# Optimization experiments

Hardware: AMD Instinct MI355X
Metric: run time of the kernel (lower is better)

## Reference

```python
import jax, jax.numpy as jnp
import numpy as np

N_NODES = 100000
N_EDGES = 1600000
IN_CH = 128
HID = 128   # 2 * out_channels
OUT_CH = 64


def setup_inputs() -> dict:
    key = jax.random.key(0)
    k1, k2, k3, k4, k5, k6 = jax.random.split(key, 6)
    x = jax.random.normal(k1, (N_NODES, IN_CH), dtype=jnp.float32)
    edge_index = jax.random.randint(k2, (2, N_EDGES), 0, N_NODES, dtype=jnp.int64)
    W1 = jax.random.normal(k3, (IN_CH, HID), dtype=jnp.float32) / np.sqrt(IN_CH)
    b1 = jax.random.normal(k4, (HID,), dtype=jnp.float32) * 0.01
    W2 = jax.random.normal(k5, (HID, OUT_CH), dtype=jnp.float32) / np.sqrt(HID)
    b2 = jax.random.normal(k6, (OUT_CH,), dtype=jnp.float32) * 0.01
    return {"x": x, "edge_index": edge_index, "W1": W1, "b1": b1, "W2": W2, "b2": b2}


def _gcn_layer(x, src, dst, norm, W, b, n_nodes):
    # GCNConv: linear transform, then normalized scatter-add aggregation + bias
    h = x @ W                                   # [N, d_out]
    msg = h[src] * norm[:, None]                # gather + edge normalize, [E+N, d_out]
    out = jax.ops.segment_sum(msg, dst, num_segments=n_nodes)
    return out + b


def reference(x, edge_index, W1, b1, W2, b2):
    n = x.shape[0]
    loop = jnp.arange(n, dtype=edge_index.dtype)
    # add self-loops (PyG GCNConv default)
    src = jnp.concatenate([edge_index[0], loop])
    dst = jnp.concatenate([edge_index[1], loop])
    # symmetric normalization deg^-1/2[src] * deg^-1/2[dst]
    deg = jax.ops.segment_sum(jnp.ones_like(dst, x.dtype), dst, num_segments=n)
    dinv = jnp.where(deg > 0, jax.lax.rsqrt(deg), 0.0)
    norm = dinv[src] * dinv[dst]

    h = jax.nn.relu(_gcn_layer(x, src, dst, norm, W1, b1, n))
    out = jax.nn.relu(_gcn_layer(h, src, dst, norm, W2, b2, n))
    return out
```

## Files before the change

### kernel.cpp

```cpp
#include <hip/hip_runtime.h>
#include <hip/hip_fp16.h>

typedef _Float16 f16x8 __attribute__((ext_vector_type(8)));
typedef float f32x4 __attribute__((ext_vector_type(4)));

#define BSH 9
#define BSZ 512
#define CAP 12288

__global__ __launch_bounds__(256) void passA(const int* __restrict__ ei,
                                             int* __restrict__ bcount, int E, int NB) {
  __shared__ int hist[256];
  int t = threadIdx.x;
  hist[t] = 0;
  __syncthreads();
  for (int e = blockIdx.x * 256 + t; e < E; e += gridDim.x * 256)
    atomicAdd(&hist[ei[E + e] >> BSH], 1);
  __syncthreads();
  if (t < NB && hist[t]) atomicAdd(&bcount[t], hist[t]);
}

__global__ __launch_bounds__(256) void scanB(const int* __restrict__ bcount,
                                             int* __restrict__ bstart,
                                             int* __restrict__ bfill, int NB, int E) {
  __shared__ int s[256];
  int t = threadIdx.x;
  int v = (t < NB) ? bcount[t] : 0;
  s[t] = v;
  __syncthreads();
  for (int off = 1; off < 256; off <<= 1) {
    int add = (t >= off) ? s[t - off] : 0;
    __syncthreads();
    s[t] += add;
    __syncthreads();
  }
  if (t < NB) {
    int ex = s[t] - v;
    bstart[t] = ex;
    bfill[t] = ex;
  }
  if (t == 0) bstart[NB] = E;
}

template <int NC, int NWC, bool IN_F16, bool SCALE>
__device__ __forceinline__ void gemm_mfma_body(
    const void* __restrict__ Xv, const float* __restrict__ W,
    const float* __restrict__ dinv, _Float16* __restrict__ G, int nrows, int bid,
    _Float16* Bs) {
  int t = threadIdx.x;
  {
    int n = t % NC;
    int kh = (t / NC) * (NC / 2);
    constexpr int NBLK = (NC / 2) / 8;
#pragma unroll
    for (int b = 0; b < NBLK; ++b) {
      f16x8 tmp;
#pragma unroll
      for (int j = 0; j < 8; ++j)
        tmp[j] = (_Float16)W[(size_t)(kh + b * 8 + j) * NC + n];
      *(f16x8*)(&Bs[n * 136 + kh + b * 8]) = tmp;
    }
  }
  __syncthreads();

  int w = t >> 6, lane = t & 63;
  int m = lane & 15, q = lane >> 4;
  int wr = (w / NWC) * 64, wc = (w % NWC) * 64;
  int row0 = bid * ((4 / NWC) * 64);

  f32x4 acc[4][4];
#pragma unroll
  for (int rt = 0; rt < 4; ++rt)
#pragma unroll
    for (int ct = 0; ct < 4; ++ct)
#pragma unroll
      for (int qq = 0; qq < 4; ++qq) acc[rt][ct][qq] = 0.f;

#pragma unroll
  for (int kc = 0; kc < 4; ++kc) {
    int kbase = kc * 32 + q * 8;
    f16x8 af[4];
#pragma unroll
    for (int rt = 0; rt < 4; ++rt) {
      int row = row0 + wr + rt * 16 + m;
      if constexpr (IN_F16) {
        f16x8 a = {0, 0, 0, 0, 0, 0, 0, 0};
        if (row < nrows) a = *(const f16x8*)((const _Float16*)Xv + (size_t)row * 128 + kbase);
        af[rt] = a;
      } else {
        float4 x0 = {0, 0, 0, 0}, x1 = {0, 0, 0, 0};
        if (row < nrows) {
          const float* Xf = (const float*)Xv;
          x0 = *(const float4*)(Xf + (size_t)row * 128 + kbase);
          x1 = *(const float4*)(Xf + (size_t)row * 128 + kbase + 4);
        }
        f16x8 a;
        a[0] = (_Float16)x0.x; a[1] = (_Float16)x0.y;
        a[2] = (_Float16)x0.z; a[3] = (_Float16)x0.w;
        a[4] = (_Float16)x1.x; a[5] = (_Float16)x1.y;
        a[6] = (_Float16)x1.z; a[7] = (_Float16)x1.w;
        af[rt] = a;
      }
    }
    f16x8 bf[4];
#pragma unroll
    for (int ct = 0; ct < 4; ++ct) {
      int n = wc + ct * 16 + m;
      bf[ct] = *(f16x8*)(&Bs[n * 136 + kbase]);
    }
#pragma unroll
    for (int rt = 0; rt < 4; ++rt)
#pragma unroll
      for (int ct = 0; ct < 4; ++ct)
        acc[rt][ct] = __builtin_amdgcn_mfma_f32_16x16x32_f16(af[rt], bf[ct],
                                                             acc[rt][ct], 0, 0, 0);
  }
#pragma unroll
  for (int rt = 0; rt < 4; ++rt) {
#pragma unroll
    for (int r = 0; r < 4; ++r) {
      int row = row0 + wr + rt * 16 + q * 4 + r;
      if (row < nrows) {
        float d = SCALE ? dinv[row] : 1.f;
#pragma unroll
        for (int ct = 0; ct < 4; ++ct) {
          int col = wc + ct * 16 + m;
          G[(size_t)row * NC + col] = (_Float16)(acc[rt][ct][r] * d);
        }
      }
    }
  }
}

__global__ __launch_bounds__(256) void fused_gemm_passB(
    const float* __restrict__ X, const float* __restrict__ W1,
    _Float16* __restrict__ G, int nrows, int GB,
    const int* __restrict__ ei, int* __restrict__ bfill,
    unsigned int* __restrict__ pairs, int E, int PB) {
  __shared__ char smem[128 * 136 * 2];
  int g = blockIdx.x;
  int M2 = 2 * (GB < PB ? GB : PB);
  bool is_gemm;
  int bid;
  if (g < M2) { is_gemm = (g & 1) == 0; bid = g >> 1; }
  else        { is_gemm = (GB > PB);    bid = g - M2 + (GB < PB ? GB : PB); }
  if (is_gemm) {
    gemm_mfma_body<128, 2, false, false>(X, W1, nullptr, G, nrows, bid,
                                         (_Float16*)smem);
  } else {
    int* hist = (int*)smem;
    int* gbase = (int*)(smem + 1024);
    int t = threadIdx.x;
    hist[t] = 0;
    __syncthreads();
    int d[8], s[8], lp[8], bb[8];
    int base = bid * 2048;
#pragma unroll
    for (int u = 0; u < 8; ++u) {
      int e = base + u * 256 + t;
      if (e < E) {
        d[u] = ei[E + e];
        s[u] = ei[e];
        bb[u] = d[u] >> BSH;
        lp[u] = atomicAdd(&hist[bb[u]], 1);
      } else {
        bb[u] = -1;
      }
    }
    __syncthreads();
    if (hist[t]) gbase[t] = atomicAdd(&bfill[t], hist[t]);
    __syncthreads();
#pragma unroll
    for (int u = 0; u < 8; ++u)
      if (bb[u] >= 0)
        pairs[gbase[bb[u]] + lp[u]] =
            ((unsigned int)(d[u] & (BSZ - 1)) << 17) | (unsigned int)s[u];
  }
}

__global__ __launch_bounds__(512) void passC(const unsigned int* __restrict__ pairs,
                                             const int* __restrict__ bstart,
                                             int* __restrict__ rowstart,
                                             int* __restrict__ deg,
                                             float* __restrict__ dinv,
                                             int* __restrict__ csr, int N) {
  __shared__ int hcnt[BSZ];
  __shared__ int lfill[BSZ];
  __shared__ int ss[512];
  __shared__ int lcsr[CAP];
  int b = blockIdx.x;
  int t = threadIdx.x;
  int lo = bstart[b], hi = bstart[b + 1];
  int cnt = hi - lo;
  int nbase = b << BSH;
  hcnt[t] = 0;
  __syncthreads();
  for (int k = lo + t; k < hi; k += 512)
    atomicAdd(&hcnt[(pairs[k] >> 17) & (BSZ - 1)], 1);
  __syncthreads();
  int v = hcnt[t];
  ss[t] = v;
  __syncthreads();
  for (int off = 1; off < 512; off <<= 1) {
    int add = (t >= off) ? ss[t - off] : 0;
    __syncthreads();
    ss[t] += add;
    __syncthreads();
  }
  int ex = ss[t] - v;
  lfill[t] = ex;
  int node = nbase + t;
  if (node < N) {
    rowstart[node] = lo + ex;
    deg[node] = v;
    dinv[node] = rsqrtf((float)(v + 1));
  }
  __syncthreads();
  bool fits = (cnt <= CAP);
  for (int k = lo + t; k < hi; k += 512) {
    unsigned int p = pairs[k];
    int pos = atomicAdd(&lfill[(p >> 17) & (BSZ - 1)], 1);
    int src = (int)(p & 0x1FFFFu);
    if (fits) lcsr[pos] = src;
    else      csr[lo + pos] = src;
  }
  __syncthreads();
  if (fits)
    for (int k = t; k < cnt; k += 512) csr[lo + k] = lcsr[k];
}

__global__ __launch_bounds__(256) void agg128_g2(
    const __half* __restrict__ G, const int* __restrict__ csr,
    const int* __restrict__ rowstart, const int* __restrict__ deg,
    const float* __restrict__ dinv, const float* __restrict__ b1,
    const float* __restrict__ W2, __half* __restrict__ g2, int n, int ngroups) {
  __shared__ __half2 W2s[64 * 64];
  __shared__ float2 hbuf[4][64];
  int t = threadIdx.x;
  for (int idx = t; idx < 4096; idx += 256) {
    int j = idx >> 6, c = idx & 63;
    W2s[idx] = __floats2half2_rn(W2[(size_t)(2 * j) * 64 + c],
                                 W2[(size_t)(2 * j + 1) * 64 + c]);
  }
  __syncthreads();

  int w = t >> 6, lane = t & 63;
  const __half2* Gp = (const __half2*)G;
  for (int grp = blockIdx.x; grp < ngroups; grp += gridDim.x) {
    int wid = grp * 4 + w;
    if (wid < n) {
      int i = __builtin_amdgcn_readfirstlane(wid);
      float di = dinv[i];
      float2 g = __half22float2(Gp[(size_t)i * 64 + lane]);
      float2 a = {di * g.x, di * g.y};
      int s = rowstart[i];
      int d = deg[i];
      int k = 0;
      for (; k + 3 < d; k += 4) {
        int s0 = csr[s + k], s1 = csr[s + k + 1];
        int s2 = csr[s + k + 2], s3 = csr[s + k + 3];
        float w0 = dinv[s0], w1 = dinv[s1], w2 = dinv[s2], w3 = dinv[s3];
        float2 v0 = __half22float2(Gp[(size_t)s0 * 64 + lane]);
        float2 v1 = __half22float2(Gp[(size_t)s1 * 64 + lane]);
        float2 v2 = __half22float2(Gp[(size_t)s2 * 64 + lane]);
        float2 v3 = __half22float2(Gp[(size_t)s3 * 64 + lane]);
        a.x = fmaf(w0, v0.x, a.x); a.y = fmaf(w0, v0.y, a.y);
        a.x = fmaf(w1, v1.x, a.x); a.y = fmaf(w1, v1.y, a.y);
        a.x = fmaf(w2, v2.x, a.x); a.y = fmaf(w2, v2.y, a.y);
        a.x = fmaf(w3, v3.x, a.x); a.y = fmaf(w3, v3.y, a.y);
      }
      for (; k < d; ++k) {
        int s0 = csr[s + k];
        float w0 = dinv[s0];
        float2 v0 = __half22float2(Gp[(size_t)s0 * 64 + lane]);
        a.x = fmaf(w0, v0.x, a.x); a.y = fmaf(w0, v0.y, a.y);
      }
      float2 b = ((const float2*)b1)[lane];
      float hx = fmaxf(fmaf(di, a.x, b.x), 0.f);
      float hy = fmaxf(fmaf(di, a.y, b.y), 0.f);
      hbuf[w][lane] = make_float2(hx, hy);
      float acc = 0.f;
#pragma unroll 8
      for (int j = 0; j < 64; ++j) {
        float2 h = hbuf[w][j];
        float2 wf = __half22float2(W2s[j * 64 + lane]);
        acc = fmaf(h.x, wf.x, fmaf(h.y, wf.y, acc));
      }
      g2[(size_t)i * 64 + lane] = (__half)(acc * di);
    }
  }
}

__global__ __launch_bounds__(256) void agg64(
    const __half* __restrict__ G, const int* __restrict__ csr,
    const int* __restrict__ rowstart, const int* __restrict__ deg,
    const float* __restrict__ dinv, const float* __restrict__ bias,
    float* __restrict__ out, int n) {
  int wid = blockIdx.x * 4 + (threadIdx.x >> 6);
  if (wid >= n) return;
  int i = __builtin_amdgcn_readfirstlane(wid);
  int lane = threadIdx.x & 63;
  float a = __half2float(G[(size_t)i * 64 + lane]);
  int s = rowstart[i];
  int d = deg[i];
  int k = 0;
  for (; k + 3 < d; k += 4) {
    int s0 = csr[s + k], s1 = csr[s + k + 1];
    int s2 = csr[s + k + 2], s3 = csr[s + k + 3];
    float v0 = __half2float(G[(size_t)s0 * 64 + lane]);
    float v1 = __half2float(G[(size_t)s1 * 64 + lane]);
    float v2 = __half2float(G[(size_t)s2 * 64 + lane]);
    float v3 = __half2float(G[(size_t)s3 * 64 + lane]);
    a += (v0 + v1) + (v2 + v3);
  }
  for (; k < d; ++k) {
    int s0 = csr[s + k];
    a += __half2float(G[(size_t)s0 * 64 + lane]);
  }
  float o = fmaxf(fmaf(dinv[i], a, bias[lane]), 0.f);
  out[(size_t)i * 64 + lane] = o;
}

extern "C" void kernel_launch(void* const* d_in, const int* in_sizes, int n_in,
                              void* d_out, int out_size, void* d_ws, size_t ws_size,
                              hipStream_t stream) {
  const float* x  = (const float*)d_in[0];
  const int*   ei = (const int*)d_in[1];
  const float* W1 = (const float*)d_in[2];
  const float* b1 = (const float*)d_in[3];
  const float* W2 = (const float*)d_in[4];
  const float* b2 = (const float*)d_in[5];
  float* out = (float*)d_out;

  const int N = in_sizes[0] / 128;
  const int E = in_sizes[1] / 2;
  const int NB = (N + BSZ - 1) >> BSH;

  char* base = (char*)d_ws;
  size_t off = 0;
  auto alloc = [&](size_t bytes) -> void* {
    void* p = base + off;
    off += (bytes + 255) & ~(size_t)255;
    return p;
  };
  int*          bcount   = (int*)alloc(256 * 4);
  int*          bstart   = (int*)alloc(260 * 4);
  int*          bfill    = (int*)alloc(256 * 4);
  int*          deg      = (int*)alloc((size_t)N * 4);
  int*          rowstart = (int*)alloc((size_t)N * 4);
  float*        dinv     = (float*)alloc((size_t)N * 4);
  int*          csr      = (int*)alloc((size_t)E * 4);
  unsigned int* pairs    = (unsigned int*)alloc((size_t)E * 4);
  __half*       g1       = (__half*)alloc((size_t)N * 128 * 2);
  __half*       g2       = (__half*)alloc((size_t)N * 64 * 2);

  hipMemsetAsync(bcount, 0, 256 * 4, stream);
  passA<<<512, 256, 0, stream>>>(ei, bcount, E, NB);
  scanB<<<1, 256, 0, stream>>>(bcount, bstart, bfill, NB, E);

  int GB = (N + 127) / 128;
  int PB = (E + 2047) / 2048;
  fused_gemm_passB<<<GB + PB, 256, 0, stream>>>(x, W1, (_Float16*)g1, N, GB, ei,
                                                bfill, pairs, E, PB);
  passC<<<NB, 512, 0, stream>>>(pairs, bstart, rowstart, deg, dinv, csr, N);

  int ngroups = (N + 3) / 4;
  agg128_g2<<<2048, 256, 0, stream>>>(g1, csr, rowstart, deg, dinv, b1, W2, g2,
                                      N, ngroups);
  agg64<<<ngroups, 256, 0, stream>>>(g2, csr, rowstart, deg, dinv, b2, out, N);
}
```

Measured before the change: 301.2 us.

## Use MFMA for layer-2 transform and split agg64 edges across half-waves

The layer-1 aggregation kernel now handles 16 nodes per wave and stages their hidden rows in shared memory as fp16. It then computes the 128x64 W2 product with MFMA 16x16x32 instructions instead of a per-node scalar dot loop over shared memory. The layer-2 aggregation reads half2 pairs, with the two half-waves processing different edges, and combines them with a cross-lane shuffle. This aims to cut the ALU/LDS cost of the dense transform and to raise memory-level parallelism in the gather. The trade-off is fp16 rounding of the hidden activations and a per-wave serial loop over 16 nodes, which could reduce latency hiding.

```diff
diff --git a/kernel.cpp b/kernel.cpp
--- a/kernel.cpp
+++ b/kernel.cpp
@@ -229,32 +229,48 @@
     for (int k = t; k < cnt; k += 512) csr[lo + k] = lcsr[k];
 }
 
-__global__ __launch_bounds__(256) void agg128_g2(
+#define HPAD 144
+__global__ __launch_bounds__(256) void agg128_mm(
     const __half* __restrict__ G, const int* __restrict__ csr,
     const int* __restrict__ rowstart, const int* __restrict__ deg,
     const float* __restrict__ dinv, const float* __restrict__ b1,
-    const float* __restrict__ W2, __half* __restrict__ g2, int n, int ngroups) {
-  __shared__ __half2 W2s[64 * 64];
-  __shared__ float2 hbuf[4][64];
+    const float* __restrict__ W2, _Float16* __restrict__ g2, int N) {
+  __shared__ _Float16 Ws[64 * 136];
+  __shared__ _Float16 Hs[4][16 * HPAD];
   int t = threadIdx.x;
-  for (int idx = t; idx < 4096; idx += 256) {
-    int j = idx >> 6, c = idx & 63;
-    W2s[idx] = __floats2half2_rn(W2[(size_t)(2 * j) * 64 + c],
-                                 W2[(size_t)(2 * j + 1) * 64 + c]);
+  {
+    int n = t & 63;
+    int kh = (t >> 6) * 32;
+#pragma unroll
+    for (int b = 0; b < 4; ++b) {
+      f16x8 tmp;
+#pragma unroll
+      for (int j = 0; j < 8; ++j)
+        tmp[j] = (_Float16)W2[(size_t)(kh + b * 8 + j) * 64 + n];
+      *(f16x8*)(&Ws[n * 136 + kh + b * 8]) = tmp;
+    }
   }
   __syncthreads();
 
   int w = t >> 6, lane = t & 63;
+  int m = lane & 15, q = lane >> 4;
   const __half2* Gp = (const __half2*)G;
-  for (int grp = blockIdx.x; grp < ngroups; grp += gridDim.x) {
-    int wid = grp * 4 + w;
-    if (wid < n) {
-      int i = __builtin_amdgcn_readfirstlane(wid);
-      float di = dinv[i];
-      float2 g = __half22float2(Gp[(size_t)i * 64 + lane]);
+  float2 bb = ((const float2*)b1)[lane];
+  int node0 = (blockIdx.x * 4 + w) * 16;
+  if (node0 >= N) return;
+
+  _Float16* H = Hs[w];
+#pragma unroll 1
+  for (int u = 0; u < 16; ++u) {
+    int i = node0 + u;
+    float2 h = {0.f, 0.f};
+    if (i < N) {
+      int ii = __builtin_amdgcn_readfirstlane(i);
+      float di = dinv[ii];
+      float2 g = __half22float2(Gp[(size_t)ii * 64 + lane]);
       float2 a = {di * g.x, di * g.y};
-      int s = rowstart[i];
-      int d = deg[i];
+      int s = rowstart[ii];
+      int d = deg[ii];
       int k = 0;
       for (; k + 3 < d; k += 4) {
         int s0 = csr[s + k], s1 = csr[s + k + 1];
@@ -275,18 +291,36 @@
         float2 v0 = __half22float2(Gp[(size_t)s0 * 64 + lane]);
         a.x = fmaf(w0, v0.x, a.x); a.y = fmaf(w0, v0.y, a.y);
       }
-      float2 b = ((const float2*)b1)[lane];
-      float hx = fmaxf(fmaf(di, a.x, b.x), 0.f);
-      float hy = fmaxf(fmaf(di, a.y, b.y), 0.f);
-      hbuf[w][lane] = make_float2(hx, hy);
-      float acc = 0.f;
-#pragma unroll 8
-      for (int j = 0; j < 64; ++j) {
-        float2 h = hbuf[w][j];
-        float2 wf = __half22float2(W2s[j * 64 + lane]);
-        acc = fmaf(h.x, wf.x, fmaf(h.y, wf.y, acc));
-      }
-      g2[(size_t)i * 64 + lane] = (__half)(acc * di);
+      h.x = fmaxf(fmaf(di, a.x, bb.x), 0.f);
+      h.y = fmaxf(fmaf(di, a.y, bb.y), 0.f);
+    }
+    H[u * HPAD + 2 * lane]     = (_Float16)h.x;
+    H[u * HPAD + 2 * lane + 1] = (_Float16)h.y;
+  }
+
+  f32x4 acc[4];
+#pragma unroll
+  for (int ct = 0; ct < 4; ++ct)
+#pragma unroll
+    for (int qq = 0; qq < 4; ++qq) acc[ct][qq] = 0.f;
+#pragma unroll
+  for (int kc = 0; kc < 4; ++kc) {
+    int kb = kc * 32 + q * 8;
+    f16x8 af = *(f16x8*)(&H[m * HPAD + kb]);
+#pragma unroll
+    for (int ct = 0; ct < 4; ++ct) {
+      f16x8 bf = *(f16x8*)(&Ws[(ct * 16 + m) * 136 + kb]);
+      acc[ct] = __builtin_amdgcn_mfma_f32_16x16x32_f16(af, bf, acc[ct], 0, 0, 0);
+    }
+  }
+#pragma unroll
+  for (int r = 0; r < 4; ++r) {
+    int i = node0 + q * 4 + r;
+    if (i < N) {
+      float di = dinv[i];
+#pragma unroll
+      for (int ct = 0; ct < 4; ++ct)
+        g2[(size_t)i * 64 + ct * 16 + m] = (_Float16)(acc[ct][r] * di);
     }
   }
 }
@@ -300,25 +334,33 @@
   if (wid >= n) return;
   int i = __builtin_amdgcn_readfirstlane(wid);
   int lane = threadIdx.x & 63;
-  float a = __half2float(G[(size_t)i * 64 + lane]);
-  int s = rowstart[i];
+  int e2 = lane >> 5, f = lane & 31;
+  const __half2* Gp = (const __half2*)G;
+  int r0 = rowstart[i];
   int d = deg[i];
-  int k = 0;
-  for (; k + 3 < d; k += 4) {
-    int s0 = csr[s + k], s1 = csr[s + k + 1];
-    int s2 = csr[s + k + 2], s3 = csr[s + k + 3];
-    float v0 = __half2float(G[(size_t)s0 * 64 + lane]);
-    float v1 = __half2float(G[(size_t)s1 * 64 + lane]);
-    float v2 = __half2float(G[(size_t)s2 * 64 + lane]);
-    float v3 = __half2float(G[(size_t)s3 * 64 + lane]);
-    a += (v0 + v1) + (v2 + v3);
-  }
-  for (; k < d; ++k) {
-    int s0 = csr[s + k];
-    a += __half2float(G[(size_t)s0 * 64 + lane]);
-  }
-  float o = fmaxf(fmaf(dinv[i], a, bias[lane]), 0.f);
-  out[(size_t)i * 64 + lane] = o;
+  float2 acc = {0.f, 0.f};
+  for (int k = 0; k < d; k += 4) {
+    int kA = k + e2, kB = k + 2 + e2;
+    int iA = i, iB = i;
+    float wA = 0.f, wB = 0.f;
+    if (kA < d) { iA = csr[r0 + kA]; wA = 1.f; }
+    if (kB < d) { iB = csr[r0 + kB]; wB = 1.f; }
+    float2 vA = __half22float2(Gp[(size_t)iA * 32 + f]);
+    float2 vB = __half22float2(Gp[(size_t)iB * 32 + f]);
+    acc.x = fmaf(wA, vA.x, acc.x); acc.y = fmaf(wA, vA.y, acc.y);
+    acc.x = fmaf(wB, vB.x, acc.x); acc.y = fmaf(wB, vB.y, acc.y);
+  }
+  acc.x += __shfl_xor(acc.x, 32);
+  acc.y += __shfl_xor(acc.y, 32);
+  if (e2 == 0) {
+    float di = dinv[i];
+    float2 g = __half22float2(Gp[(size_t)i * 32 + f]);
+    float2 b = ((const float2*)bias)[f];
+    float2 o;
+    o.x = fmaxf(fmaf(di, g.x + acc.x, b.x), 0.f);
+    o.y = fmaxf(fmaf(di, g.y + acc.y, b.y), 0.f);
+    ((float2*)out)[(size_t)i * 32 + f] = o;
+  }
 }
 
 extern "C" void kernel_launch(void* const* d_in, const int* in_sizes, int n_in,
@@ -364,8 +406,9 @@
                                                 bfill, pairs, E, PB);
   passC<<<NB, 512, 0, stream>>>(pairs, bstart, rowstart, deg, dinv, csr, N);
 
-  int ngroups = (N + 3) / 4;
-  agg128_g2<<<2048, 256, 0, stream>>>(g1, csr, rowstart, deg, dinv, b1, W2, g2,
-                                      N, ngroups);
-  agg64<<<ngroups, 256, 0, stream>>>(g2, csr, rowstart, deg, dinv, b2, out, N);
-}
+  int nmm = (N + 63) / 64;
+  agg128_mm<<<nmm, 256, 0, stream>>>(g1, csr, rowstart, deg, dinv, b1, W2,
+                                     (_Float16*)g2, N);
+  int ng = (N + 3) / 4;
+  agg64<<<ng, 256, 0, stream>>>(g2, csr, rowstart, deg, dinv, b2, out, N);
+}
```

Result: slower. 342.4 us (+13.7%).
